# Optimization experiments

Measured on AMD Instinct MI355X. Metric: run time of the kernel, lower is better.

The kernel has to match this reference:

```python
import jax, jax.numpy as jnp
import numpy as np

# Window-batch of 16x16 windows from a U-Net stage
B, C, H, W = 128, 128, 16, 16
HEADS = 8
EQK, EV = 128, 512      # embed_dim_qk, embed_dim_v (embed_dim=512, ratio=4)
L = H * W               # tokens per window (stride=1)


def _conv3x3(x, w, b):
    # NCHW 3x3 conv, padding 1
    out = jax.lax.conv_general_dilated(x, w, (1, 1), ((1, 1), (1, 1)),
                                       dimension_numbers=('NCHW', 'OIHW', 'NCHW'))
    return out + b[None, :, None, None]


def _pos_att(q, wq, bq, wk, bk, wv, bv, wo, bo, gamma):
    # MultiHeadAttention2D_POS, stride=1 -> conv_q/k/v are 1x1 convs
    hd, hdv = EQK // HEADS, EV // HEADS

    def proj(x, w, bias, d):
        y = jnp.einsum('bchw,ec->behw', x, w) + bias[None, :, None, None]
        return y.reshape(B, HEADS, d, L).transpose(0, 1, 3, 2)  # (B,h,L,d)

    pq = proj(q, wq, bq, hd)
    pk = proj(q, wk, bk, hd)
    pv = proj(q, wv, bv, hdv)
    attn = jax.nn.softmax(jnp.einsum('bhqd,bhkd->bhqk', pq, pk) * hd ** -0.5, axis=-1)
    out = jnp.einsum('bhqk,bhkd->bhqd', attn, pv)
    out = out.transpose(0, 1, 3, 2).reshape(B, EV, H, W)
    out = _conv3x3(out, wo, bo)             # proj_out: 3x3 conv EV->C
    return q + out * gamma                  # gamma-scaled residual


def _cha_att(q, wq, bq, wk, bk, wv, bv, wo, bo, gamma):
    # MultiHeadAttention2D_CHA: depthwise 1x1 grouped convs (channel multiplier = HEADS),
    # attention over the CHANNEL axis. Faithfully reproduces torch's reshape of the
    # group-major (c*HEADS+h) channel layout into (B, heads, C, L).
    def dwproj(x, w, bias):
        y = (x[:, :, None] * w.reshape(C, HEADS)[None, :, :, None, None]
             + bias.reshape(C, HEADS)[None, :, :, None, None])
        return y.reshape(B, C * HEADS, H, W).reshape(B, HEADS, C, L)

    pq = dwproj(q, wq, bq)
    pk = dwproj(q, wk, bk)
    pv = dwproj(q, wv, bv)
    attn = jax.nn.softmax(jnp.einsum('bhcl,bhdl->bhcd', pq, pk) * L ** -0.5, axis=-1)
    out = jnp.einsum('bhcd,bhdl->bhcl', attn, pv)      # (B,h,C,L)
    out = out.reshape(B, HEADS * C, H, W)
    # proj_out: grouped 1x1 ConvTranspose (== grouped 1x1 conv): sum each HEADS-sized group
    out = (out.reshape(B, C, HEADS, H, W)
           * wo.reshape(C, HEADS)[None, :, :, None, None]).sum(2) + bo[None, :, None, None]
    return q + out * gamma


def _forward(qkv_pos, qkv_cha,
             pos_wq, pos_bq, pos_wk, pos_bk, pos_wv, pos_bv, pos_wo, pos_bo, gamma_pos,
             cha_wq, cha_bq, cha_wk, cha_bk, cha_wv, cha_bv, cha_wo, cha_bo, gamma_cha,
             fuse_w, fuse_b):
    out_pos = _pos_att(qkv_pos, pos_wq, pos_bq, pos_wk, pos_bk, pos_wv, pos_bv,
                       pos_wo, pos_bo, gamma_pos)
    out_cha = _cha_att(qkv_cha, cha_wq, cha_bq, cha_wk, cha_bk, cha_wv, cha_bv,
                       cha_wo, cha_bo, gamma_cha)
    out = (out_pos + out_cha) * 0.5          # att_fusion='add' (slides=0 -> full slices)
    return _conv3x3(out, fuse_w, fuse_b)     # conv_out (Dropout2d is identity at eval)


def setup_inputs() -> dict:
    key = jax.random.key(0)
    ks = jax.random.split(key, 24)
    n = lambda k, shape, s=0.05: jax.random.normal(k, shape, dtype=jnp.float32) * s
    return {
        'qkv_pos': jax.random.normal(ks[0], (B, C, H, W), jnp.float32),
        'qkv_cha': jax.random.normal(ks[1], (B, C, H, W), jnp.float32),
        'pos_wq': n(ks[2], (EQK, C)), 'pos_bq': n(ks[3], (EQK,)),
        'pos_wk': n(ks[4], (EQK, C)), 'pos_bk': n(ks[5], (EQK,)),
        'pos_wv': n(ks[6], (EV, C)), 'pos_bv': n(ks[7], (EV,)),
        'pos_wo': n(ks[8], (C, EV, 3, 3)), 'pos_bo': n(ks[9], (C,)),
        'gamma_pos': jnp.array(0.1, jnp.float32),
        'cha_wq': n(ks[10], (C * HEADS,)), 'cha_bq': n(ks[11], (C * HEADS,)),
        'cha_wk': n(ks[12], (C * HEADS,)), 'cha_bk': n(ks[13], (C * HEADS,)),
        'cha_wv': n(ks[14], (C * HEADS,)), 'cha_bv': n(ks[15], (C * HEADS,)),
        'cha_wo': n(ks[16], (C * HEADS,)), 'cha_bo': n(ks[17], (C,)),
        'gamma_cha': jnp.array(0.1, jnp.float32),
        'fuse_w': n(ks[18], (C, C, 3, 3)), 'fuse_b': n(ks[19], (C,)),
    }


def reference(qkv_pos, qkv_cha,
              pos_wq, pos_bq, pos_wk, pos_bk, pos_wv, pos_bv, pos_wo, pos_bo, gamma_pos,
              cha_wq, cha_bq, cha_wk, cha_bk, cha_wv, cha_bv, cha_wo, cha_bo, gamma_cha,
              fuse_w, fuse_b):
    return _forward(qkv_pos, qkv_cha,
                    pos_wq, pos_bq, pos_wk, pos_bk, pos_wv, pos_bv, pos_wo, pos_bo, gamma_pos,
                    cha_wq, cha_bq, cha_wk, cha_bk, cha_wv, cha_bv, cha_wo, cha_bo, gamma_cha,
                    fuse_w, fuse_b)
```

## Files before the change

kernel.cpp:

```cpp
#include <hip/hip_runtime.h>
#include <cstdint>
#include <cstddef>

typedef unsigned short ushort_t;
typedef unsigned int uint_t;
typedef __attribute__((ext_vector_type(8))) short bf16x8;
typedef __attribute__((ext_vector_type(4))) float f32x4;

#define NB 128
#define NC 128
#define NL 256
#define NH 8
#define HD 16
#define HDV 64
#define NEV 512
#define PHALF 4194304

__device__ __forceinline__ ushort_t f2bf(float f) {
    uint_t u = __float_as_uint(f);
    u += 0x7fffu + ((u >> 16) & 1u);
    return (ushort_t)(u >> 16);
}
__device__ __forceinline__ float bf2f(ushort_t s) {
    return __uint_as_float(((uint_t)s) << 16);
}
__device__ __forceinline__ uint_t pack2(float lo, float hi) {
    uint_t r;
    asm("v_cvt_pk_bf16_f32 %0, %1, %2" : "=v"(r) : "v"(lo), "v"(hi));
    return r;
}

template<int CIN>
__global__ __launch_bounds__(256) void k_wpack(const float* __restrict__ w,
                                               short* __restrict__ wp) {
    int idx = blockIdx.x * 256 + threadIdx.x;
    if (idx >= CIN * 1152) return;
    int j    = idx & 7;
    int lane = (idx >> 3) & 63;
    int frag = idx >> 9;
    int rt   = frag & 7;
    int tap  = (frag >> 3) % 9;
    int ch   = frag / 72;
    int co   = rt * 16 + (lane & 15);
    int g    = lane >> 4;
    int ci   = ch * 32 + g * 8 + j;
    wp[idx] = (short)f2bf(w[((size_t)co * CIN + ci) * 9 + tap]);
}

template<int E>
__global__ __launch_bounds__(256) void k_wpack_qkv(const float* __restrict__ w,
                                                   short* __restrict__ wp) {
    int idx = blockIdx.x * 256 + threadIdx.x;
    if (idx >= E * 128) return;
    int j    = idx & 7;
    int lane = (idx >> 3) & 63;
    int ch   = (idx >> 9) & 3;
    int rt   = idx >> 11;
    int n = lane & 15, g = lane >> 4;
    wp[idx] = (short)f2bf(w[(size_t)(rt*16 + n)*128 + ch*32 + g*8 + j]);
}

__global__ __launch_bounds__(256) void k_xpose(const float* __restrict__ x,
                                               ushort_t* __restrict__ xbf) {
    const int half = blockIdx.x, b = blockIdx.y, t = threadIdx.x;
    const float* src = x + (size_t)b*NC*NL + (size_t)half*64*NL + t;
    uint_t* dst = (uint_t*)(xbf + ((size_t)b*NL + t)*NC + half*64);
    #pragma unroll
    for (int k8 = 0; k8 < 8; ++k8) {
        uint4 u;
        u.x = pack2(src[(k8*8+0)*NL], src[(k8*8+1)*NL]);
        u.y = pack2(src[(k8*8+2)*NL], src[(k8*8+3)*NL]);
        u.z = pack2(src[(k8*8+4)*NL], src[(k8*8+5)*NL]);
        u.w = pack2(src[(k8*8+6)*NL], src[(k8*8+7)*NL]);
        *(uint4*)(dst + k8*4) = u;
    }
}

__global__ __launch_bounds__(256) void k_pos_mfma(
    const ushort_t* __restrict__ xbf,
    const short* __restrict__ wpq, const short* __restrict__ wpk,
    const short* __restrict__ wpv,
    const float* __restrict__ bq, const float* __restrict__ bk,
    const float* __restrict__ bv,
    ushort_t* __restrict__ att)
{
    const int h = blockIdx.x, b = blockIdx.y;
    const int t = threadIdx.x;
    const int lane = t & 63, w = t >> 6;
    const int n = lane & 15, g = lane >> 4;

    __shared__ __align__(16) short lds[23552];

    const f32x4 z4 = {0.f, 0.f, 0.f, 0.f};
    f32x4 qacc[4], kacc[4], vacc[4][4];
    #pragma unroll
    for (int ct = 0; ct < 4; ++ct) { qacc[ct] = z4; kacc[ct] = z4; }
    #pragma unroll
    for (int vt = 0; vt < 4; ++vt)
        #pragma unroll
        for (int ct = 0; ct < 4; ++ct) vacc[vt][ct] = z4;

    const ushort_t* xr = xbf + ((size_t)(b*NL + w*64 + n))*NC;

    #pragma unroll 2
    for (int ch = 0; ch < 4; ++ch) {
        bf16x8 xb[4];
        #pragma unroll
        for (int ct = 0; ct < 4; ++ct)
            xb[ct] = *(const bf16x8*)(xr + ct*16*NC + ch*32 + g*8);
        const size_t fo = ((size_t)((h*4 + ch)*64) + lane) * 8;
        {
            bf16x8 aq = *(const bf16x8*)(wpq + fo);
            #pragma unroll
            for (int ct = 0; ct < 4; ++ct)
                qacc[ct] = __builtin_amdgcn_mfma_f32_16x16x32_bf16(aq, xb[ct], qacc[ct], 0, 0, 0);
        }
        {
            bf16x8 ak = *(const bf16x8*)(wpk + fo);
            #pragma unroll
            for (int ct = 0; ct < 4; ++ct)
                kacc[ct] = __builtin_amdgcn_mfma_f32_16x16x32_bf16(ak, xb[ct], kacc[ct], 0, 0, 0);
        }
        #pragma unroll
        for (int vt = 0; vt < 4; ++vt) {
            bf16x8 av = *(const bf16x8*)(wpv + ((size_t)((((h*4 + vt)*4) + ch)*64) + lane) * 8);
            #pragma unroll
            for (int ct = 0; ct < 4; ++ct)
                vacc[vt][ct] = __builtin_amdgcn_mfma_f32_16x16x32_bf16(xb[ct], av, vacc[vt][ct], 0, 0, 0);
        }
    }

    uint_t qu01[4], qu23[4];
    {
        float bqv[4], bkv[4];
        #pragma unroll
        for (int r = 0; r < 4; ++r) {
            bqv[r] = bq[h*16 + g*4 + r];
            bkv[r] = bk[h*16 + g*4 + r];
        }
        #pragma unroll
        for (int ct = 0; ct < 4; ++ct) {
            qu01[ct] = pack2(qacc[ct][0] + bqv[0], qacc[ct][1] + bqv[1]);
            qu23[ct] = pack2(qacc[ct][2] + bqv[2], qacc[ct][3] + bqv[3]);
            uint2 kp;
            kp.x = pack2(kacc[ct][0] + bkv[0], kacc[ct][1] + bkv[1]);
            kp.y = pack2(kacc[ct][2] + bkv[2], kacc[ct][3] + bkv[3]);
            *(uint2*)&lds[(w*64 + ct*16 + n)*16 + g*4] = kp;
        }
        #pragma unroll
        for (int vt = 0; vt < 4; ++vt) {
            const float bvv = bv[h*64 + vt*16 + n];
            #pragma unroll
            for (int ct = 0; ct < 4; ++ct) {
                uint2 vp;
                vp.x = pack2(vacc[vt][ct][0] + bvv, vacc[vt][ct][1] + bvv);
                vp.y = pack2(vacc[vt][ct][2] + bvv, vacc[vt][ct][3] + bvv);
                *(uint2*)&lds[6656 + (vt*16 + n)*264 + w*64 + ct*16 + g*4] = vp;
            }
        }
    }
    __syncthreads();

    const int a0 = (n + 32*(g & 1)) * 4;
    #pragma unroll 1
    for (int qt = 0; qt < 4; ++qt) {
        union { uint_t u[4]; bf16x8 v; } qfu;
        qfu.u[0] = (uint_t)__builtin_amdgcn_ds_bpermute(a0,      (int)qu01[qt]);
        qfu.u[1] = (uint_t)__builtin_amdgcn_ds_bpermute(a0,      (int)qu23[qt]);
        qfu.u[2] = (uint_t)__builtin_amdgcn_ds_bpermute(a0 + 64, (int)qu01[qt]);
        qfu.u[3] = (uint_t)__builtin_amdgcn_ds_bpermute(a0 + 64, (int)qu23[qt]);
        if (g >= 2) { qfu.u[0] = 0; qfu.u[1] = 0; qfu.u[2] = 0; qfu.u[3] = 0; }
        bf16x8 qf = qfu.v;

        f32x4 s[16];
        #pragma unroll
        for (int kt = 0; kt < 16; ++kt) {
            bf16x8 kf = (bf16x8){0,0,0,0,0,0,0,0};
            if (g < 2) kf = *(const bf16x8*)&lds[(kt*16 + n)*16 + g*8];
            s[kt] = __builtin_amdgcn_mfma_f32_16x16x32_bf16(kf, qf, z4, 0, 0, 0);
        }
        float den = 0.f;
        #pragma unroll
        for (int kt = 0; kt < 16; ++kt)
            #pragma unroll
            for (int r = 0; r < 4; ++r) {
                float e = exp2f(s[kt][r] * 0.36067376022224085f);
                s[kt][r] = e;
                den += e;
            }
        den += __shfl_xor(den, 16);
        den += __shfl_xor(den, 32);
        const float inv = 1.f / den;

        f32x4 oacc[4] = {z4, z4, z4, z4};
        #pragma unroll
        for (int c2 = 0; c2 < 8; ++c2) {
            #pragma unroll
            for (int u = 0; u < 2; ++u) {
                const int kt = 2*c2 + u;
                uint2 pp;
                pp.x = pack2(s[kt][0], s[kt][1]);
                pp.y = pack2(s[kt][2], s[kt][3]);
                *(uint2*)&lds[4096 + w*640 + n*40 + u*16 + g*4] = pp;
            }
            bf16x8 pf = *(const bf16x8*)&lds[4096 + w*640 + n*40 + g*8];
            #pragma unroll
            for (int vt = 0; vt < 4; ++vt) {
                bf16x8 av = *(const bf16x8*)&lds[6656 + (vt*16 + n)*264 + c2*32 + g*8];
                oacc[vt] = __builtin_amdgcn_mfma_f32_16x16x32_bf16(av, pf, oacc[vt], 0, 0, 0);
            }
        }
        ushort_t* ap = att + (((size_t)b*NL + (w*64 + qt*16 + n))*NEV + h*HDV + g*4);
        #pragma unroll
        for (int vt = 0; vt < 4; ++vt) {
            uint2 op;
            op.x = pack2(oacc[vt][0]*inv, oacc[vt][1]*inv);
            op.y = pack2(oacc[vt][2]*inv, oacc[vt][3]*inv);
            *(uint2*)(ap + vt*16) = op;
        }
    }
}

__global__ __launch_bounds__(256, 3) void k_conv_ci(
    const ushort_t* __restrict__ att, const short* __restrict__ wp,
    ushort_t* __restrict__ P)
{
    const int kc = blockIdx.x >> 1, lh = blockIdx.x & 1, b = blockIdx.y;
    const int t = threadIdx.x;
    const int lane = t & 63, w = t >> 6;
    const int wr = w >> 1, wc = w & 1;
    const int n = lane & 15, gl = lane >> 4;
    const int y0 = lh * 8;

    __shared__ __align__(16) short ims[2][5760];

    {
        bf16x8 z = {0,0,0,0,0,0,0,0};
        bf16x8* p = (bf16x8*)&ims[0][0];
        for (int i = t; i < 1440; i += 256) p[i] = z;
    }

    f32x4 acc[4][4];
    #pragma unroll
    for (int i = 0; i < 4; ++i)
        #pragma unroll
        for (int j = 0; j < 4; ++j) acc[i][j] = (f32x4){0.f,0.f,0.f,0.f};

    const int gg1 = t & 3,        xx1 = (t >> 2) & 15,        yp1 = t >> 6;
    const int id2 = t + 256;
    const int gg2 = id2 & 3,      xx2 = (id2 >> 2) & 15,      yp2 = id2 >> 6;
    const int id3 = t + 512;
    const int gg3 = id3 & 3,      xx3 = (id3 >> 2) & 15,      yp3 = id3 >> 6;
    const bool has3 = (t < 128);
    const int y1 = y0 - 1 + yp1, y2 = y0 - 1 + yp2, y3 = y0 - 1 + yp3;
    const bool ok1 = (y1 >= 0) && (y1 < 16);
    const bool ok2 = (y2 >= 0) && (y2 < 16);
    const bool ok3 = has3 && (y3 >= 0) && (y3 < 16);
    const ushort_t* src1 = att + ((size_t)(b*NL + y1*16 + xx1))*NEV + kc*256 + gg1*8;
    const ushort_t* src2 = att + ((size_t)(b*NL + y2*16 + xx2))*NEV + kc*256 + gg2*8;
    const ushort_t* src3 = att + ((size_t)(b*NL + y3*16 + xx3))*NEV + kc*256 + gg3*8;
    const int slot1 = ((yp1*4 + gg1)*18 + xx1 + 1) * 8;
    const int slot2 = ((yp2*4 + gg2)*18 + xx2 + 1) * 8;
    const int slot3 = ((yp3*4 + gg3)*18 + xx3 + 1) * 8;

    bf16x8 v1 = {0,0,0,0,0,0,0,0}, v2 = v1, v3 = v1;
    if (ok1) v1 = *(const bf16x8*)src1;
    if (ok2) v2 = *(const bf16x8*)src2;
    if (ok3) v3 = *(const bf16x8*)src3;
    __syncthreads();

    #pragma unroll 1
    for (int ch = 0; ch < 8; ++ch) {
        short* buf = &ims[ch & 1][0];
        *(bf16x8*)&buf[slot1] = v1;
        *(bf16x8*)&buf[slot2] = v2;
        if (has3) *(bf16x8*)&buf[slot3] = v3;
        if (ch < 7) {
            if (ok1) v1 = *(const bf16x8*)(src1 + (ch + 1) * 32);
            if (ok2) v2 = *(const bf16x8*)(src2 + (ch + 1) * 32);
            if (ok3) v3 = *(const bf16x8*)(src3 + (ch + 1) * 32);
        }
        __syncthreads();
        #pragma unroll
        for (int tap = 0; tap < 9; ++tap) {
            const int dy = tap / 3, dx = tap % 3;
            bf16x8 Bf[4];
            #pragma unroll
            for (int ct = 0; ct < 4; ++ct)
                Bf[ct] = *(const bf16x8*)&buf[(((wc*4 + ct + dy)*4 + gl)*18 + n + dx) * 8];
            bf16x8 Af[4];
            #pragma unroll
            for (int rt = 0; rt < 4; ++rt)
                Af[rt] = *(const bf16x8*)(wp +
                    ((size_t)(((kc*8 + ch)*9 + tap)*8 + wr*4 + rt)) * 512 + lane*8);
            #pragma unroll
            for (int rt = 0; rt < 4; ++rt)
                #pragma unroll
                for (int ct = 0; ct < 4; ++ct)
                    acc[rt][ct] = __builtin_amdgcn_mfma_f32_16x16x32_bf16(
                        Af[rt], Bf[ct], acc[rt][ct], 0, 0, 0);
        }
    }

    ushort_t* Pb = P + (size_t)kc * PHALF + (size_t)b * NL * NC;
    #pragma unroll
    for (int rt = 0; rt < 4; ++rt) {
        const int co0 = wr*64 + rt*16 + gl*4;
        #pragma unroll
        for (int ct = 0; ct < 4; ++ct) {
            const int l = lh*128 + wc*64 + ct*16 + n;
            uint2 u;
            u.x = pack2(acc[rt][ct][0], acc[rt][ct][1]);
            u.y = pack2(acc[rt][ct][2], acc[rt][ct][3]);
            *(uint2*)(Pb + (size_t)l*NC + co0) = u;
        }
    }
}

__global__ __launch_bounds__(512, 2) void k_conv_co(
    const float* __restrict__ comb, const short* __restrict__ wp,
    const float* __restrict__ bias, float* __restrict__ out)
{
    const int kc = blockIdx.x, b = blockIdx.y;
    const int t = threadIdx.x;
    const int lane = t & 63, w = t >> 6;
    const int wr = w & 1, wc = w >> 1;
    const int n = lane & 15, gl = lane >> 4;

    __shared__ __align__(16) short ims[2][10368];

    {
        bf16x8 z = {0,0,0,0,0,0,0,0};
        bf16x8* p = (bf16x8*)&ims[0][0];
        for (int i = t; i < 2592; i += 512) p[i] = z;
    }

    f32x4 acc[2][4];
    #pragma unroll
    for (int i = 0; i < 2; ++i)
        #pragma unroll
        for (int j = 0; j < 4; ++j) acc[i][j] = (f32x4){0.f,0.f,0.f,0.f};

    const int g1 = t & 3, x1 = (t >> 2) & 15, y1 = t >> 6;
    const float* s1 = comb + ((size_t)(b*NL + y1*16 + x1))*NC + g1*8;
    const float* s2 = comb + ((size_t)(b*NL + (y1+8)*16 + x1))*NC + g1*8;
    const int slot1 = (((y1+1)*4 + g1)*18 + x1 + 1) * 8;
    const int slot2 = (((y1+9)*4 + g1)*18 + x1 + 1) * 8;

    float4 a1 = *(const float4*)s1,       b1_ = *(const float4*)(s1 + 4);
    float4 a2 = *(const float4*)s2,       b2_ = *(const float4*)(s2 + 4);
    __syncthreads();

    #pragma unroll 1
    for (int ch = 0; ch < 4; ++ch) {
        short* buf = &ims[ch & 1][0];
        uint4 w1, w2;
        w1.x = pack2(a1.x, a1.y);   w1.y = pack2(a1.z, a1.w);
        w1.z = pack2(b1_.x, b1_.y); w1.w = pack2(b1_.z, b1_.w);
        w2.x = pack2(a2.x, a2.y);   w2.y = pack2(a2.z, a2.w);
        w2.z = pack2(b2_.x, b2_.y); w2.w = pack2(b2_.z, b2_.w);
        *(uint4*)&buf[slot1] = w1;
        *(uint4*)&buf[slot2] = w2;
        if (ch < 3) {
            a1  = *(const float4*)(s1 + (ch+1)*32);
            b1_ = *(const float4*)(s1 + (ch+1)*32 + 4);
            a2  = *(const float4*)(s2 + (ch+1)*32);
            b2_ = *(const float4*)(s2 + (ch+1)*32 + 4);
        }
        __syncthreads();
        #pragma unroll
        for (int tap = 0; tap < 9; ++tap) {
            const int dy = tap / 3, dx = tap % 3;
            bf16x8 Bf[4];
            #pragma unroll
            for (int ct = 0; ct < 4; ++ct)
                Bf[ct] = *(const bf16x8*)&buf[((((wc*4 + ct + dy)*4) + gl)*18 + n + dx) * 8];
            bf16x8 Af[2];
            #pragma unroll
            for (int rt = 0; rt < 2; ++rt)
                Af[rt] = *(const bf16x8*)(wp +
                    ((size_t)((ch*9 + tap)*8 + kc*4 + wr*2 + rt)) * 512 + lane*8);
            #pragma unroll
            for (int rt = 0; rt < 2; ++rt)
                #pragma unroll
                for (int ct = 0; ct < 4; ++ct)
                    acc[rt][ct] = __builtin_amdgcn_mfma_f32_16x16x32_bf16(
                        Af[rt], Bf[ct], acc[rt][ct], 0, 0, 0);
        }
    }

    #pragma unroll
    for (int rt = 0; rt < 2; ++rt) {
        const int co0 = kc*64 + wr*32 + rt*16 + gl*4;
        const float c0 = bias[co0+0], c1 = bias[co0+1],
                    c2 = bias[co0+2], c3 = bias[co0+3];
        #pragma unroll
        for (int ct = 0; ct < 4; ++ct) {
            const int l = wc*64 + ct*16 + n;
            f32x4 a = acc[rt][ct];
            out[((size_t)b*NC + co0+0)*NL + l] = c0 + a[0];
            out[((size_t)b*NC + co0+1)*NL + l] = c1 + a[1];
            out[((size_t)b*NC + co0+2)*NL + l] = c2 + a[2];
            out[((size_t)b*NC + co0+3)*NL + l] = c3 + a[3];
        }
    }
}

#define NLP 260
__global__ __launch_bounds__(256) void k_cha(
    const float* __restrict__ xc,
    const float* __restrict__ cwq, const float* __restrict__ cbq,
    const float* __restrict__ cwk, const float* __restrict__ cbk,
    const float* __restrict__ cwv, const float* __restrict__ cbv,
    const float* __restrict__ cwo, const float* __restrict__ cbo,
    const float* __restrict__ gamma,
    const ushort_t* __restrict__ P, const float* __restrict__ qpos,
    const float* __restrict__ pbo, const float* __restrict__ gpos,
    float* __restrict__ comb)
{
    const int h = blockIdx.x, b = blockIdx.y, t = threadIdx.x;
    __shared__ float qh[16][NLP];
    __shared__ float G_s[16][17];
    __shared__ float S_s[16];
    __shared__ float wq_s[128], bq_s[128], wk_s[128], bk_s[128], wv_s[128], bv_s[128];
    __shared__ float A_s[128][17];
    __shared__ float B_s[128];
    __shared__ float M_s[16][17];
    __shared__ float c_s[16];

    #pragma unroll
    for (int j = 0; j < 16; ++j)
        qh[j][t] = xc[((size_t)b*NC + h*16 + j)*NL + t];
    if (t < 128) {
        const int k = h*128 + t;
        wq_s[t] = cwq[k]; bq_s[t] = cbq[k];
        wk_s[t] = cwk[k]; bk_s[t] = cbk[k];
        wv_s[t] = cwv[k]; bv_s[t] = cbv[k];
    }
    __syncthreads();
    {
        const int i = t >> 4, j = t & 15;
        const float4* qi = (const float4*)qh[i];
        const float4* qj = (const float4*)qh[j];
        float gg = 0.f;
        for (int l4 = 0; l4 < NL/4; ++l4) {
            float4 a = qi[l4], c = qj[l4];
            gg = fmaf(a.x,c.x,fmaf(a.y,c.y,fmaf(a.z,c.z,fmaf(a.w,c.w,gg))));
        }
        G_s[i][j] = gg;
    }
    if (t < 16) {
        const float4* qi = (const float4*)qh[t];
        float s = 0.f;
        for (int l4 = 0; l4 < NL/4; ++l4) { float4 a = qi[l4]; s += a.x + a.y + a.z + a.w; }
        S_s[t] = s;
    }
    __syncthreads();
    if (t < 128) {
        const int c2 = t, cg = c2 >> 3;
        const float wqc = wq_s[c2], bqc = bq_s[c2];
        float Pv[16];
        #pragma unroll
        for (int j = 0; j < 16; ++j) Pv[j] = wqc*G_s[cg][j] + bqc*S_s[j];
        const float Qc = wqc*S_s[cg] + bqc*256.0f;
        float mx = -3.0e38f;
        #pragma unroll
        for (int dg = 0; dg < 16; ++dg) {
            #pragma unroll
            for (int dj = 0; dj < 8; ++dj) {
                const int d = dg*8 + dj;
                float s = wk_s[d]*Pv[dg] + bk_s[d]*Qc;
                mx = fmaxf(mx, s);
            }
        }
        float A[16];
        #pragma unroll
        for (int j = 0; j < 16; ++j) A[j] = 0.f;
        float Bv = 0.f, den = 0.f;
        #pragma unroll
        for (int dg = 0; dg < 16; ++dg) {
            #pragma unroll
            for (int dj = 0; dj < 8; ++dj) {
                const int d = dg*8 + dj;
                float s = wk_s[d]*Pv[dg] + bk_s[d]*Qc;
                float e = __expf((s - mx) * 0.0625f);
                den += e;
                A[dg] = fmaf(e, wv_s[d], A[dg]);
                Bv = fmaf(e, bv_s[d], Bv);
            }
        }
        const float inv = 1.f / den;
        #pragma unroll
        for (int j = 0; j < 16; ++j) A_s[c2][j] = A[j]*inv;
        B_s[c2] = Bv*inv;
    }
    __syncthreads();
    {
        const int cl = t >> 4, j = t & 15;
        const int cp = h*16 + cl;
        float m = 0.f;
        #pragma unroll
        for (int hp = 0; hp < 8; ++hp)
            m = fmaf(cwo[cp*8+hp], A_s[cl*8+hp][j], m);
        M_s[cl][j] = m;
        if (j == 0) {
            float cc = cbo[cp];
            #pragma unroll
            for (int hp = 0; hp < 8; ++hp)
                cc = fmaf(cwo[cp*8+hp], B_s[cl*8+hp], cc);
            c_s[cl] = cc;
        }
    }
    __syncthreads();
    {
        const float g  = gamma[0];
        const float gp = gpos[0];
        const int l = t;
        float av[16];
        #pragma unroll
        for (int cl = 0; cl < 16; ++cl) {
            float a = c_s[cl];
            #pragma unroll
            for (int j = 0; j < 16; ++j)
                a = fmaf(M_s[cl][j], qh[j][l], a);
            av[cl] = a;
        }
        const ushort_t* p0 = P + ((size_t)b*NL + l)*NC + h*16;
        const ushort_t* p1 = p0 + PHALF;
        const float* qp = qpos + ((size_t)b*NC + h*16)*NL + l;
        float4* cp4 = (float4*)(comb + ((size_t)b*NL + l)*NC + h*16);
        #pragma unroll
        for (int q = 0; q < 4; ++q) {
            uint2 u0 = *(const uint2*)(p0 + 4*q);
            uint2 u1 = *(const uint2*)(p1 + 4*q);
            float s0 = bf2f((ushort_t)(u0.x & 0xffffu)) + bf2f((ushort_t)(u1.x & 0xffffu));
            float s1 = bf2f((ushort_t)(u0.x >> 16))     + bf2f((ushort_t)(u1.x >> 16));
            float s2 = bf2f((ushort_t)(u0.y & 0xffffu)) + bf2f((ushort_t)(u1.y & 0xffffu));
            float s3 = bf2f((ushort_t)(u0.y >> 16))     + bf2f((ushort_t)(u1.y >> 16));
            float4 c;
            c.x = 0.5f*(qp[(4*q+0)*NL] + gp*(pbo[h*16+4*q+0] + s0) + qh[4*q+0][l] + g*av[4*q+0]);
            c.y = 0.5f*(qp[(4*q+1)*NL] + gp*(pbo[h*16+4*q+1] + s1) + qh[4*q+1][l] + g*av[4*q+1]);
            c.z = 0.5f*(qp[(4*q+2)*NL] + gp*(pbo[h*16+4*q+2] + s2) + qh[4*q+2][l] + g*av[4*q+2]);
            c.w = 0.5f*(qp[(4*q+3)*NL] + gp*(pbo[h*16+4*q+3] + s3) + qh[4*q+3][l] + g*av[4*q+3]);
            cp4[q] = c;
        }
    }
}

extern "C" void kernel_launch(void* const* d_in, const int* in_sizes, int n_in,
                              void* d_out, int out_size, void* d_ws, size_t ws_size,
                              hipStream_t stream)
{
    const float* qpos = (const float*)d_in[0];
    const float* qcha = (const float*)d_in[1];
    const float* pwq  = (const float*)d_in[2];
    const float* pbq  = (const float*)d_in[3];
    const float* pwk  = (const float*)d_in[4];
    const float* pbk  = (const float*)d_in[5];
    const float* pwv  = (const float*)d_in[6];
    const float* pbv  = (const float*)d_in[7];
    const float* pwo  = (const float*)d_in[8];
    const float* pbo  = (const float*)d_in[9];
    const float* gpos = (const float*)d_in[10];
    const float* cwq  = (const float*)d_in[11];
    const float* cbq  = (const float*)d_in[12];
    const float* cwk  = (const float*)d_in[13];
    const float* cbk  = (const float*)d_in[14];
    const float* cwv  = (const float*)d_in[15];
    const float* cbv  = (const float*)d_in[16];
    const float* cwo  = (const float*)d_in[17];
    const float* cbo  = (const float*)d_in[18];
    const float* gcha = (const float*)d_in[19];
    const float* fw   = (const float*)d_in[20];
    const float* fb   = (const float*)d_in[21];
    float* outp = (float*)d_out;

    char* ws = (char*)d_ws;
    ushort_t* att  = (ushort_t*)ws;
    float*    comb = (float*)ws;
    ushort_t* P    = (ushort_t*)(ws + 33554432);
    ushort_t* xbf  = (ushort_t*)(ws + 33554432);
    short*    wp1  = (short*)(ws + 50331648);
    short*    wp2  = (short*)(ws + 51511296);
    short*    wpq  = (short*)(ws + 51806208);
    short*    wpk  = (short*)(ws + 51838976);
    short*    wpv  = (short*)(ws + 51871744);

    k_wpack<NEV><<<dim3((NEV*1152 + 255)/256), 256, 0, stream>>>(pwo, wp1);
    k_wpack<NC ><<<dim3((NC *1152 + 255)/256), 256, 0, stream>>>(fw,  wp2);
    k_wpack_qkv<128><<<dim3(64),  256, 0, stream>>>(pwq, wpq);
    k_wpack_qkv<128><<<dim3(64),  256, 0, stream>>>(pwk, wpk);
    k_wpack_qkv<512><<<dim3(256), 256, 0, stream>>>(pwv, wpv);

    k_xpose<<<dim3(2, NB), 256, 0, stream>>>(qpos, xbf);
    k_pos_mfma<<<dim3(NH, NB), 256, 0, stream>>>(xbf, wpq, wpk, wpv,
                                                 pbq, pbk, pbv, att);
    k_conv_ci<<<dim3(4, NB), 256, 0, stream>>>(att, wp1, P);
    k_cha<<<dim3(NH, NB), 256, 0, stream>>>(qcha, cwq, cbq, cwk, cbk, cwv, cbv,
                                            cwo, cbo, gcha,
                                            P, qpos, pbo, gpos, comb);
    k_conv_co<<<dim3(2, NB), 512, 0, stream>>>(comb, wp2, fb, outp);
}
```

Baseline: 181.6 us.

## Split pos-attention over 8 waves and conv_co over spatial halves

k_pos_mfma now runs 512 threads per block, so each of 8 waves projects and attends over 32 query tokens instead of 64. The K/V LDS regions are resized to fit 256 keys across 8 waves. k_conv_co is restructured from 512-thread blocks covering the full 16x16 image into 256-thread blocks covering 8-row halves with halo loads and boundary masks, doubling the grid. The goal is more waves in flight and smaller per-block work, at the cost of redundant halo loads and duplicated weight fetches.

```diff
diff --git a/kernel.cpp b/kernel.cpp
--- a/kernel.cpp
+++ b/kernel.cpp
@@ -76,7 +76,7 @@
     }
 }
 
-__global__ __launch_bounds__(256) void k_pos_mfma(
+__global__ __launch_bounds__(512, 4) void k_pos_mfma(
     const ushort_t* __restrict__ xbf,
     const short* __restrict__ wpq, const short* __restrict__ wpk,
     const short* __restrict__ wpv,
@@ -89,48 +89,48 @@
     const int lane = t & 63, w = t >> 6;
     const int n = lane & 15, g = lane >> 4;
 
-    __shared__ __align__(16) short lds[23552];
+    __shared__ __align__(16) short lds[26112];
 
     const f32x4 z4 = {0.f, 0.f, 0.f, 0.f};
-    f32x4 qacc[4], kacc[4], vacc[4][4];
-    #pragma unroll
-    for (int ct = 0; ct < 4; ++ct) { qacc[ct] = z4; kacc[ct] = z4; }
+    f32x4 qacc[2], kacc[2], vacc[4][2];
+    #pragma unroll
+    for (int ct = 0; ct < 2; ++ct) { qacc[ct] = z4; kacc[ct] = z4; }
     #pragma unroll
     for (int vt = 0; vt < 4; ++vt)
         #pragma unroll
-        for (int ct = 0; ct < 4; ++ct) vacc[vt][ct] = z4;
-
-    const ushort_t* xr = xbf + ((size_t)(b*NL + w*64 + n))*NC;
+        for (int ct = 0; ct < 2; ++ct) vacc[vt][ct] = z4;
+
+    const ushort_t* xr = xbf + ((size_t)(b*NL + w*32 + n))*NC;
 
     #pragma unroll 2
     for (int ch = 0; ch < 4; ++ch) {
-        bf16x8 xb[4];
-        #pragma unroll
-        for (int ct = 0; ct < 4; ++ct)
+        bf16x8 xb[2];
+        #pragma unroll
+        for (int ct = 0; ct < 2; ++ct)
             xb[ct] = *(const bf16x8*)(xr + ct*16*NC + ch*32 + g*8);
         const size_t fo = ((size_t)((h*4 + ch)*64) + lane) * 8;
         {
             bf16x8 aq = *(const bf16x8*)(wpq + fo);
             #pragma unroll
-            for (int ct = 0; ct < 4; ++ct)
+            for (int ct = 0; ct < 2; ++ct)
                 qacc[ct] = __builtin_amdgcn_mfma_f32_16x16x32_bf16(aq, xb[ct], qacc[ct], 0, 0, 0);
         }
         {
             bf16x8 ak = *(const bf16x8*)(wpk + fo);
             #pragma unroll
-            for (int ct = 0; ct < 4; ++ct)
+            for (int ct = 0; ct < 2; ++ct)
                 kacc[ct] = __builtin_amdgcn_mfma_f32_16x16x32_bf16(ak, xb[ct], kacc[ct], 0, 0, 0);
         }
         #pragma unroll
         for (int vt = 0; vt < 4; ++vt) {
             bf16x8 av = *(const bf16x8*)(wpv + ((size_t)((((h*4 + vt)*4) + ch)*64) + lane) * 8);
             #pragma unroll
-            for (int ct = 0; ct < 4; ++ct)
+            for (int ct = 0; ct < 2; ++ct)
                 vacc[vt][ct] = __builtin_amdgcn_mfma_f32_16x16x32_bf16(xb[ct], av, vacc[vt][ct], 0, 0, 0);
         }
     }
 
-    uint_t qu01[4], qu23[4];
+    uint_t qu01[2], qu23[2];
     {
         float bqv[4], bkv[4];
         #pragma unroll
@@ -139,23 +139,23 @@
             bkv[r] = bk[h*16 + g*4 + r];
         }
         #pragma unroll
-        for (int ct = 0; ct < 4; ++ct) {
+        for (int ct = 0; ct < 2; ++ct) {
             qu01[ct] = pack2(qacc[ct][0] + bqv[0], qacc[ct][1] + bqv[1]);
             qu23[ct] = pack2(qacc[ct][2] + bqv[2], qacc[ct][3] + bqv[3]);
             uint2 kp;
             kp.x = pack2(kacc[ct][0] + bkv[0], kacc[ct][1] + bkv[1]);
             kp.y = pack2(kacc[ct][2] + bkv[2], kacc[ct][3] + bkv[3]);
-            *(uint2*)&lds[(w*64 + ct*16 + n)*16 + g*4] = kp;
+            *(uint2*)&lds[(w*32 + ct*16 + n)*16 + g*4] = kp;
         }
         #pragma unroll
         for (int vt = 0; vt < 4; ++vt) {
             const float bvv = bv[h*64 + vt*16 + n];
             #pragma unroll
-            for (int ct = 0; ct < 4; ++ct) {
+            for (int ct = 0; ct < 2; ++ct) {
                 uint2 vp;
                 vp.x = pack2(vacc[vt][ct][0] + bvv, vacc[vt][ct][1] + bvv);
                 vp.y = pack2(vacc[vt][ct][2] + bvv, vacc[vt][ct][3] + bvv);
-                *(uint2*)&lds[6656 + (vt*16 + n)*264 + w*64 + ct*16 + g*4] = vp;
+                *(uint2*)&lds[9216 + (vt*16 + n)*264 + w*32 + ct*16 + g*4] = vp;
             }
         }
     }
@@ -163,7 +163,7 @@
 
     const int a0 = (n + 32*(g & 1)) * 4;
     #pragma unroll 1
-    for (int qt = 0; qt < 4; ++qt) {
+    for (int qt = 0; qt < 2; ++qt) {
         union { uint_t u[4]; bf16x8 v; } qfu;
         qfu.u[0] = (uint_t)__builtin_amdgcn_ds_bpermute(a0,      (int)qu01[qt]);
         qfu.u[1] = (uint_t)__builtin_amdgcn_ds_bpermute(a0,      (int)qu23[qt]);
@@ -206,11 +206,11 @@
             bf16x8 pf = *(const bf16x8*)&lds[4096 + w*640 + n*40 + g*8];
             #pragma unroll
             for (int vt = 0; vt < 4; ++vt) {
-                bf16x8 av = *(const bf16x8*)&lds[6656 + (vt*16 + n)*264 + c2*32 + g*8];
+                bf16x8 av = *(const bf16x8*)&lds[9216 + (vt*16 + n)*264 + c2*32 + g*8];
                 oacc[vt] = __builtin_amdgcn_mfma_f32_16x16x32_bf16(av, pf, oacc[vt], 0, 0, 0);
             }
         }
-        ushort_t* ap = att + (((size_t)b*NL + (w*64 + qt*16 + n))*NEV + h*HDV + g*4);
+        ushort_t* ap = att + (((size_t)b*NL + (w*32 + qt*16 + n))*NEV + h*HDV + g*4);
         #pragma unroll
         for (int vt = 0; vt < 4; ++vt) {
             uint2 op;
@@ -317,22 +317,23 @@
     }
 }
 
-__global__ __launch_bounds__(512, 2) void k_conv_co(
+__global__ __launch_bounds__(256, 3) void k_conv_co(
     const float* __restrict__ comb, const short* __restrict__ wp,
     const float* __restrict__ bias, float* __restrict__ out)
 {
-    const int kc = blockIdx.x, b = blockIdx.y;
+    const int kc = blockIdx.x >> 1, lh = blockIdx.x & 1, b = blockIdx.y;
     const int t = threadIdx.x;
     const int lane = t & 63, w = t >> 6;
-    const int wr = w & 1, wc = w >> 1;
+    const int wr = w >> 1, wc = w & 1;
     const int n = lane & 15, gl = lane >> 4;
-
-    __shared__ __align__(16) short ims[2][10368];
+    const int y0 = lh * 8;
+
+    __shared__ __align__(16) short ims[2][5760];
 
     {
         bf16x8 z = {0,0,0,0,0,0,0,0};
         bf16x8* p = (bf16x8*)&ims[0][0];
-        for (int i = t; i < 2592; i += 512) p[i] = z;
+        for (int i = t; i < 1440; i += 256) p[i] = z;
     }
 
     f32x4 acc[2][4];
@@ -341,31 +342,47 @@
         #pragma unroll
         for (int j = 0; j < 4; ++j) acc[i][j] = (f32x4){0.f,0.f,0.f,0.f};
 
-    const int g1 = t & 3, x1 = (t >> 2) & 15, y1 = t >> 6;
-    const float* s1 = comb + ((size_t)(b*NL + y1*16 + x1))*NC + g1*8;
-    const float* s2 = comb + ((size_t)(b*NL + (y1+8)*16 + x1))*NC + g1*8;
-    const int slot1 = (((y1+1)*4 + g1)*18 + x1 + 1) * 8;
-    const int slot2 = (((y1+9)*4 + g1)*18 + x1 + 1) * 8;
-
-    float4 a1 = *(const float4*)s1,       b1_ = *(const float4*)(s1 + 4);
-    float4 a2 = *(const float4*)s2,       b2_ = *(const float4*)(s2 + 4);
+    const int gg1 = t & 3,        xx1 = (t >> 2) & 15,        yp1 = t >> 6;
+    const int id2 = t + 256;
+    const int gg2 = id2 & 3,      xx2 = (id2 >> 2) & 15,      yp2 = id2 >> 6;
+    const int id3 = t + 512;
+    const int gg3 = id3 & 3,      xx3 = (id3 >> 2) & 15,      yp3 = id3 >> 6;
+    const bool has3 = (t < 128);
+    const int y1 = y0 - 1 + yp1, y2 = y0 - 1 + yp2, y3 = y0 - 1 + yp3;
+    const bool ok1 = (y1 >= 0) && (y1 < 16);
+    const bool ok2 = (y2 >= 0) && (y2 < 16);
+    const bool ok3 = has3 && (y3 >= 0) && (y3 < 16);
+    const float* s1 = comb + ((size_t)(b*NL + y1*16 + xx1))*NC + gg1*8;
+    const float* s2 = comb + ((size_t)(b*NL + y2*16 + xx2))*NC + gg2*8;
+    const float* s3 = comb + ((size_t)(b*NL + y3*16 + xx3))*NC + gg3*8;
+    const int slot1 = ((yp1*4 + gg1)*18 + xx1 + 1) * 8;
+    const int slot2 = ((yp2*4 + gg2)*18 + xx2 + 1) * 8;
+    const int slot3 = ((yp3*4 + gg3)*18 + xx3 + 1) * 8;
+
+    float4 f1a, f1b, f2a, f2b, f3a, f3b;
+    f1a = f1b = f2a = f2b = f3a = f3b = (float4){0.f,0.f,0.f,0.f};
+    if (ok1) { f1a = *(const float4*)s1; f1b = *(const float4*)(s1 + 4); }
+    if (ok2) { f2a = *(const float4*)s2; f2b = *(const float4*)(s2 + 4); }
+    if (ok3) { f3a = *(const float4*)s3; f3b = *(const float4*)(s3 + 4); }
     __syncthreads();
 
     #pragma unroll 1
     for (int ch = 0; ch < 4; ++ch) {
         short* buf = &ims[ch & 1][0];
-        uint4 w1, w2;
-        w1.x = pack2(a1.x, a1.y);   w1.y = pack2(a1.z, a1.w);
-        w1.z = pack2(b1_.x, b1_.y); w1.w = pack2(b1_.z, b1_.w);
-        w2.x = pack2(a2.x, a2.y);   w2.y = pack2(a2.z, a2.w);
-        w2.z = pack2(b2_.x, b2_.y); w2.w = pack2(b2_.z, b2_.w);
+        uint4 w1, w2, w3;
+        w1.x = pack2(f1a.x, f1a.y);  w1.y = pack2(f1a.z, f1a.w);
+        w1.z = pack2(f1b.x, f1b.y);  w1.w = pack2(f1b.z, f1b.w);
+        w2.x = pack2(f2a.x, f2a.y);  w2.y = pack2(f2a.z, f2a.w);
+        w2.z = pack2(f2b.x, f2b.y);  w2.w = pack2(f2b.z, f2b.w);
+        w3.x = pack2(f3a.x, f3a.y);  w3.y = pack2(f3a.z, f3a.w);
+        w3.z = pack2(f3b.x, f3b.y);  w3.w = pack2(f3b.z, f3b.w);
         *(uint4*)&buf[slot1] = w1;
         *(uint4*)&buf[slot2] = w2;
+        if (has3) *(uint4*)&buf[slot3] = w3;
         if (ch < 3) {
-            a1  = *(const float4*)(s1 + (ch+1)*32);
-            b1_ = *(const float4*)(s1 + (ch+1)*32 + 4);
-            a2  = *(const float4*)(s2 + (ch+1)*32);
-            b2_ = *(const float4*)(s2 + (ch+1)*32 + 4);
+            if (ok1) { f1a = *(const float4*)(s1 + (ch+1)*32); f1b = *(const float4*)(s1 + (ch+1)*32 + 4); }
+            if (ok2) { f2a = *(const float4*)(s2 + (ch+1)*32); f2b = *(const float4*)(s2 + (ch+1)*32 + 4); }
+            if (ok3) { f3a = *(const float4*)(s3 + (ch+1)*32); f3b = *(const float4*)(s3 + (ch+1)*32 + 4); }
         }
         __syncthreads();
         #pragma unroll
@@ -374,7 +391,7 @@
             bf16x8 Bf[4];
             #pragma unroll
             for (int ct = 0; ct < 4; ++ct)
-                Bf[ct] = *(const bf16x8*)&buf[((((wc*4 + ct + dy)*4) + gl)*18 + n + dx) * 8];
+                Bf[ct] = *(const bf16x8*)&buf[(((wc*4 + ct + dy)*4 + gl)*18 + n + dx) * 8];
             bf16x8 Af[2];
             #pragma unroll
             for (int rt = 0; rt < 2; ++rt)
@@ -396,7 +413,7 @@
                     c2 = bias[co0+2], c3 = bias[co0+3];
         #pragma unroll
         for (int ct = 0; ct < 4; ++ct) {
-            const int l = wc*64 + ct*16 + n;
+            const int l = lh*128 + wc*64 + ct*16 + n;
             f32x4 a = acc[rt][ct];
             out[((size_t)b*NC + co0+0)*NL + l] = c0 + a[0];
             out[((size_t)b*NC + co0+1)*NL + l] = c1 + a[1];
@@ -593,11 +610,11 @@
     k_wpack_qkv<512><<<dim3(256), 256, 0, stream>>>(pwv, wpv);
 
     k_xpose<<<dim3(2, NB), 256, 0, stream>>>(qpos, xbf);
-    k_pos_mfma<<<dim3(NH, NB), 256, 0, stream>>>(xbf, wpq, wpk, wpv,
+    k_pos_mfma<<<dim3(NH, NB), 512, 0, stream>>>(xbf, wpq, wpk, wpv,
                                                  pbq, pbk, pbv, att);
     k_conv_ci<<<dim3(4, NB), 256, 0, stream>>>(att, wp1, P);
     k_cha<<<dim3(NH, NB), 256, 0, stream>>>(qcha, cwq, cbq, cwk, cbk, cwv, cbv,
                                             cwo, cbo, gcha,
                                             P, qpos, pbo, gpos, comb);
-    k_conv_co<<<dim3(2, NB), 512, 0, stream>>>(comb, wp2, fb, outp);
-}
+    k_conv_co<<<dim3(4, NB), 256, 0, stream>>>(comb, wp2, fb, outp);
+}
```

New measurement: 175.2 us. 3.6% less time.
